# Optimization experiments

Hardware: AMD Instinct MI355X
Metric: run time of the kernel (lower is better)

## Reference

```python
import jax, jax.numpy as jnp
import numpy as np

N_NODES = 50000


def _gcn_conv(x, edge_index, W, b, n_nodes):
    # PyG GCNConv: add self loops, symmetric normalization, then
    # out[dst] = sum_{src->dst} norm * (x[src] @ W) + b
    src, dst = edge_index[0], edge_index[1]
    loop = jnp.arange(n_nodes, dtype=src.dtype)
    src = jnp.concatenate([src, loop])
    dst = jnp.concatenate([dst, loop])
    deg = jax.ops.segment_sum(jnp.ones_like(src, dtype=x.dtype), dst, num_segments=n_nodes)
    dinv = jnp.where(deg > 0, jax.lax.rsqrt(deg), 0.0)
    norm = dinv[src] * dinv[dst]                      # [E+N]
    h = x @ W                                         # [N, out] dense GEMM first (in >= out here)
    msg = h[src] * norm[:, None]                      # gather + scale
    out = jax.ops.segment_sum(msg, dst, num_segments=n_nodes)  # scatter-add
    return out + b


def setup_inputs() -> dict:
    key = jax.random.key(0)
    k = jax.random.split(key, 5)
    in_c, hid_c, out_c = 128, 128, 64
    n, e = N_NODES, 800000
    x = jax.random.normal(k[0], (n, in_c), dtype=jnp.float32)
    edge_index = jax.random.randint(k[1], (2, e), 0, n, dtype=jnp.int64)
    # Glorot-ish scaled weights
    W1 = jax.random.normal(k[2], (in_c, hid_c), dtype=jnp.float32) * (1.0 / np.sqrt(in_c))
    b1 = jnp.zeros((hid_c,), dtype=jnp.float32)
    W2 = jax.random.normal(k[3], (hid_c, out_c), dtype=jnp.float32) * (1.0 / np.sqrt(hid_c))
    b2 = jnp.zeros((out_c,), dtype=jnp.float32)
    return {"x": x, "edge_index": edge_index, "W1": W1, "b1": b1, "W2": W2, "b2": b2}


def reference(x, edge_index, W1, b1, W2, b2):
    # Net.encode: conv1 -> relu -> conv2
    h = _gcn_conv(x, edge_index, W1, b1, N_NODES)
    h = jax.nn.relu(h)
    z = _gcn_conv(h, edge_index, W2, b2, N_NODES)
    return z
```

## Files before the change

### kernel.cpp

```cpp
#include <hip/hip_runtime.h>
#include <math.h>

constexpr int C_IN  = 128;
constexpr int C_HID = 128;
constexpr int C_OUT = 64;
constexpr int NREP  = 8;

typedef short bf8   __attribute__((ext_vector_type(8)));
typedef float f32x4 __attribute__((ext_vector_type(4)));

__device__ __forceinline__ int wave_incl_scan(int v, int lane) {
    #pragma unroll
    for (int off = 1; off < 64; off <<= 1) {
        int u = __shfl_up(v, off, 64);
        if (lane >= off) v += u;
    }
    return v;
}
__device__ __forceinline__ short b16(float f) {
    unsigned int u = __float_as_uint(f);
    u += 0x7FFFu + ((u >> 16) & 1u);
    return (short)(u >> 16);
}
__device__ __forceinline__ unsigned int bpack(float a, float b) {
    unsigned int ua = __float_as_uint(a), ub = __float_as_uint(b);
    ua += 0x7FFFu + ((ua >> 16) & 1u);
    ub += 0x7FFFu + ((ub >> 16) & 1u);
    return (ua >> 16) | (ub & 0xFFFF0000u);
}
__device__ __forceinline__ void acc8(float* a, const uint4 v) {
    a[0] += __uint_as_float(v.x << 16);
    a[1] += __uint_as_float(v.x & 0xFFFF0000u);
    a[2] += __uint_as_float(v.y << 16);
    a[3] += __uint_as_float(v.y & 0xFFFF0000u);
    a[4] += __uint_as_float(v.z << 16);
    a[5] += __uint_as_float(v.z & 0xFFFF0000u);
    a[6] += __uint_as_float(v.w << 16);
    a[7] += __uint_as_float(v.w & 0xFFFF0000u);
}

__global__ __launch_bounds__(256) void k_zero(int* __restrict__ p, int n4) {
    int i = blockIdx.x * 256 + threadIdx.x;
    if (i < n4) reinterpret_cast<int4*>(p)[i] = make_int4(0, 0, 0, 0);
}

__global__ __launch_bounds__(256) void k_count2r4(const int* __restrict__ dst, int e, int n,
                                                  int* __restrict__ cntr,
                                                  int* __restrict__ slot) {
    int i = blockIdx.x * 256 + threadIdx.x;
    int base = i * 4;
    if (base >= e) return;
    int r = blockIdx.x & (NREP - 1);
    int* c = cntr + (size_t)r * n;
    if (base + 3 < e) {
        int4 d4 = *reinterpret_cast<const int4*>(dst + base);
        int4 s4;
        s4.x = atomicAdd(&c[d4.x], 1);
        s4.y = atomicAdd(&c[d4.y], 1);
        s4.z = atomicAdd(&c[d4.z], 1);
        s4.w = atomicAdd(&c[d4.w], 1);
        *reinterpret_cast<int4*>(slot + base) = s4;
    } else {
        for (int q = base; q < e; ++q) slot[q] = atomicAdd(&c[dst[q]], 1);
    }
}

__global__ __launch_bounds__(256) void k_scanAB8(int* __restrict__ cntr, int n,
                                                 int* __restrict__ rowstart,
                                                 int* __restrict__ blocksum,
                                                 int* __restrict__ blockoff,
                                                 int* __restrict__ ticket,
                                                 float* __restrict__ dinv) {
    __shared__ int swave[4];
    __shared__ int amLast;
    const int tid = threadIdx.x, lane = tid & 63, w = tid >> 6;
    const int idx = blockIdx.x * 1024 + tid * 4;
    int4 c = make_int4(0, 0, 0, 0);
    if (idx + 3 < n) {
        #pragma unroll
        for (int r = 0; r < NREP; ++r) {
            int4* p = reinterpret_cast<int4*>(cntr + (size_t)r * n + idx);
            int4 t = *p;
            *p = c;
            c.x += t.x; c.y += t.y; c.z += t.z; c.w += t.w;
        }
    } else if (idx < n) {
        for (int m = idx; m < n; ++m) {
            int acc = 0;
            #pragma unroll
            for (int r = 0; r < NREP; ++r) {
                int t = cntr[(size_t)r * n + m];
                cntr[(size_t)r * n + m] = acc;
                acc += t;
            }
            int q = m - idx;
            if (q == 0) c.x = acc; else if (q == 1) c.y = acc;
            else if (q == 2) c.z = acc; else c.w = acc;
        }
    }
    if (idx + 0 < n) dinv[idx + 0] = rsqrtf((float)(c.x + 1));
    if (idx + 1 < n) dinv[idx + 1] = rsqrtf((float)(c.y + 1));
    if (idx + 2 < n) dinv[idx + 2] = rsqrtf((float)(c.z + 1));
    if (idx + 3 < n) dinv[idx + 3] = rsqrtf((float)(c.w + 1));

    const int s4 = c.x + c.y + c.z + c.w;
    const int incl = wave_incl_scan(s4, lane);
    if (lane == 63) swave[w] = incl;
    __syncthreads();
    int base = incl - s4;
    #pragma unroll
    for (int j = 0; j < 4; ++j) if (j < w) base += swave[j];

    if (idx + 3 < n) {
        int4 o;
        o.x = base;
        o.y = base + c.x;
        o.z = base + c.x + c.y;
        o.w = base + c.x + c.y + c.z;
        *reinterpret_cast<int4*>(rowstart + idx) = o;
    } else if (idx < n) {
        int acc = base;
        if (idx + 0 < n) { rowstart[idx + 0] = acc; acc += c.x; }
        if (idx + 1 < n) { rowstart[idx + 1] = acc; acc += c.y; }
        if (idx + 2 < n) { rowstart[idx + 2] = acc; acc += c.z; }
        if (idx + 3 < n) { rowstart[idx + 3] = acc; }
    }

    if (tid == 0) {
        int tot = swave[0] + swave[1] + swave[2] + swave[3];
        blocksum[blockIdx.x] = tot;
        if (blockIdx.x == gridDim.x - 1) rowstart[n] = tot;
        __threadfence();
        amLast = (atomicAdd(ticket, 1) == (int)gridDim.x - 1);
    }
    __syncthreads();
    if (amLast && tid < 64) {
        volatile int* bs = blocksum;
        const int nb = gridDim.x;
        int v = (tid < nb) ? bs[tid] : 0;
        int incl2 = wave_incl_scan(v, tid);
        if (tid < nb) blockoff[tid] = incl2 - v;
    }
}

__global__ __launch_bounds__(256) void k_fill2r4(const int* __restrict__ src,
                                                 const int* __restrict__ dst,
                                                 const int* __restrict__ slot, int e, int n,
                                                 const int* __restrict__ rowstart,
                                                 const int* __restrict__ blockoff,
                                                 const int* __restrict__ repoff,
                                                 unsigned short* __restrict__ nbr) {
    int i = blockIdx.x * 256 + threadIdx.x;
    int base = i * 4;
    if (base >= e) return;
    int r = blockIdx.x & (NREP - 1);
    const int* rep = repoff + (size_t)r * n;
    if (base + 3 < e) {
        int4 d4 = *reinterpret_cast<const int4*>(dst + base);
        int4 s4 = *reinterpret_cast<const int4*>(src + base);
        int4 t4 = *reinterpret_cast<const int4*>(slot + base);
        nbr[rowstart[d4.x] + blockoff[d4.x >> 10] + rep[d4.x] + t4.x] = (unsigned short)s4.x;
        nbr[rowstart[d4.y] + blockoff[d4.y >> 10] + rep[d4.y] + t4.y] = (unsigned short)s4.y;
        nbr[rowstart[d4.z] + blockoff[d4.z >> 10] + rep[d4.z] + t4.z] = (unsigned short)s4.z;
        nbr[rowstart[d4.w] + blockoff[d4.w >> 10] + rep[d4.w] + t4.w] = (unsigned short)s4.w;
    } else {
        for (int q = base; q < e; ++q) {
            int d = dst[q];
            nbr[rowstart[d] + blockoff[d >> 10] + rep[d] + slot[q]] = (unsigned short)src[q];
        }
    }
}

__global__ __launch_bounds__(256) void k_gemm1m(const float* __restrict__ x,
                                                const float* __restrict__ W,
                                                const float* __restrict__ dinv,
                                                unsigned short* __restrict__ h1b,
                                                int n) {
    __shared__ short wf[8 * 4 * 64 * 8];
    const int tid = threadIdx.x;

    for (int i = tid; i < 2048; i += 256) {
        const int l = i & 63, kt = (i >> 6) & 3, ct = i >> 8;
        const int krow = kt * 32 + ((l >> 4) << 3);
        const int col  = ct * 16 + (l & 15);
        const float* wp = W + (size_t)krow * C_HID + col;
        uint4 u;
        u.x = bpack(wp[0 * C_HID], wp[1 * C_HID]);
        u.y = bpack(wp[2 * C_HID], wp[3 * C_HID]);
        u.z = bpack(wp[4 * C_HID], wp[5 * C_HID]);
        u.w = bpack(wp[6 * C_HID], wp[7 * C_HID]);
        reinterpret_cast<uint4*>(wf)[i] = u;
    }
    __syncthreads();

    const int l = tid & 63, w = tid >> 6;
    const int row0 = blockIdx.x * 64 + w * 16;
    int arow = row0 + (l & 15);
    if (arow >= n) arow = n - 1;
    const float* xr = x + (size_t)arow * C_IN + ((l >> 4) << 3);

    bf8 a[4];
    #pragma unroll
    for (int kt = 0; kt < 4; ++kt) {
        float4 p0 = *reinterpret_cast<const float4*>(xr + kt * 32);
        float4 p1 = *reinterpret_cast<const float4*>(xr + kt * 32 + 4);
        bf8 t;
        t[0] = b16(p0.x); t[1] = b16(p0.y); t[2] = b16(p0.z); t[3] = b16(p0.w);
        t[4] = b16(p1.x); t[5] = b16(p1.y); t[6] = b16(p1.z); t[7] = b16(p1.w);
        a[kt] = t;
    }

    f32x4 acc[8];
    #pragma unroll
    for (int ct = 0; ct < 8; ++ct) acc[ct] = (f32x4){0.f, 0.f, 0.f, 0.f};
    const bf8* bw = reinterpret_cast<const bf8*>(wf);
    #pragma unroll
    for (int kt = 0; kt < 4; ++kt)
        #pragma unroll
        for (int ct = 0; ct < 8; ++ct)
            acc[ct] = __builtin_amdgcn_mfma_f32_16x16x32_bf16(
                a[kt], bw[(ct * 4 + kt) * 64 + l], acc[ct], 0, 0, 0);

    const int rbase = row0 + ((l >> 4) << 2);
    float dv[4];
    #pragma unroll
    for (int r = 0; r < 4; ++r) {
        int rr = rbase + r;
        dv[r] = (rr < n) ? dinv[rr] : 0.f;
    }
    #pragma unroll
    for (int ct = 0; ct < 8; ++ct) {
        const int col = ct * 16 + (l & 15);
        #pragma unroll
        for (int r = 0; r < 4; ++r) {
            int rr = rbase + r;
            if (rr < n)
                h1b[(size_t)rr * C_HID + col] = (unsigned short)b16(acc[ct][r] * dv[r]);
        }
    }
}

__global__ __launch_bounds__(256) void k_agg1b16(const uint4* __restrict__ h1v,
                                                 const int* __restrict__ rowstart,
                                                 const int* __restrict__ blockoff,
                                                 const unsigned short* __restrict__ nbr,
                                                 const float* __restrict__ dinv,
                                                 const float* __restrict__ b1,
                                                 uint4* __restrict__ actb,
                                                 int n) {
    int node = blockIdx.x * 16 + (threadIdx.x >> 4);
    if (node >= n) return;
    const int c8 = threadIdx.x & 15;
    float a8[8] = {0.f, 0.f, 0.f, 0.f, 0.f, 0.f, 0.f, 0.f};
    acc8(a8, h1v[(size_t)node * 16 + c8]);
    int j   = rowstart[node]     + blockoff[node >> 10];
    int end = rowstart[node + 1] + blockoff[(node + 1) >> 10];
    for (; j + 1 < end; j += 2) {
        int s0 = nbr[j], s1 = nbr[j + 1];
        uint4 v0 = h1v[(size_t)s0 * 16 + c8];
        uint4 v1 = h1v[(size_t)s1 * 16 + c8];
        acc8(a8, v0); acc8(a8, v1);
    }
    if (j < end) acc8(a8, h1v[(size_t)nbr[j] * 16 + c8]);
    const float sc = dinv[node];
    const float4 bb0 = reinterpret_cast<const float4*>(b1)[2 * c8 + 0];
    const float4 bb1 = reinterpret_cast<const float4*>(b1)[2 * c8 + 1];
    uint4 p;
    p.x = bpack(fmaxf(sc * a8[0] + bb0.x, 0.f), fmaxf(sc * a8[1] + bb0.y, 0.f));
    p.y = bpack(fmaxf(sc * a8[2] + bb0.z, 0.f), fmaxf(sc * a8[3] + bb0.w, 0.f));
    p.z = bpack(fmaxf(sc * a8[4] + bb1.x, 0.f), fmaxf(sc * a8[5] + bb1.y, 0.f));
    p.w = bpack(fmaxf(sc * a8[6] + bb1.z, 0.f), fmaxf(sc * a8[7] + bb1.w, 0.f));
    actb[(size_t)node * 16 + c8] = p;
}

__global__ __launch_bounds__(256) void k_gemm2m(const unsigned short* __restrict__ actb,
                                                const float* __restrict__ W2,
                                                const float* __restrict__ dinv,
                                                unsigned short* __restrict__ h2b,
                                                int n) {
    __shared__ short wf[4 * 4 * 64 * 8];
    const int tid = threadIdx.x;

    for (int i = tid; i < 1024; i += 256) {
        const int l = i & 63, kt = (i >> 6) & 3, ct = i >> 8;
        const int krow = kt * 32 + ((l >> 4) << 3);
        const int col  = ct * 16 + (l & 15);
        const float* wp = W2 + (size_t)krow * C_OUT + col;
        uint4 u;
        u.x = bpack(wp[0 * C_OUT], wp[1 * C_OUT]);
        u.y = bpack(wp[2 * C_OUT], wp[3 * C_OUT]);
        u.z = bpack(wp[4 * C_OUT], wp[5 * C_OUT]);
        u.w = bpack(wp[6 * C_OUT], wp[7 * C_OUT]);
        reinterpret_cast<uint4*>(wf)[i] = u;
    }
    __syncthreads();

    const int l = tid & 63, w = tid >> 6;
    const int row0 = blockIdx.x * 64 + w * 16;
    int arow = row0 + (l & 15);
    if (arow >= n) arow = n - 1;
    const unsigned short* ar = actb + (size_t)arow * C_HID + ((l >> 4) << 3);

    bf8 a[4];
    #pragma unroll
    for (int kt = 0; kt < 4; ++kt)
        a[kt] = *reinterpret_cast<const bf8*>(ar + kt * 32);

    f32x4 acc[4];
    #pragma unroll
    for (int ct = 0; ct < 4; ++ct) acc[ct] = (f32x4){0.f, 0.f, 0.f, 0.f};
    const bf8* bw = reinterpret_cast<const bf8*>(wf);
    #pragma unroll
    for (int kt = 0; kt < 4; ++kt)
        #pragma unroll
        for (int ct = 0; ct < 4; ++ct)
            acc[ct] = __builtin_amdgcn_mfma_f32_16x16x32_bf16(
                a[kt], bw[(ct * 4 + kt) * 64 + l], acc[ct], 0, 0, 0);

    const int rbase = row0 + ((l >> 4) << 2);
    float dv[4];
    #pragma unroll
    for (int r = 0; r < 4; ++r) {
        int rr = rbase + r;
        dv[r] = (rr < n) ? dinv[rr] : 0.f;
    }
    #pragma unroll
    for (int ct = 0; ct < 4; ++ct) {
        const int col = ct * 16 + (l & 15);
        #pragma unroll
        for (int r = 0; r < 4; ++r) {
            int rr = rbase + r;
            if (rr < n)
                h2b[(size_t)rr * C_OUT + col] = (unsigned short)b16(acc[ct][r] * dv[r]);
        }
    }
}

__global__ __launch_bounds__(256) void k_agg2b(const uint4* __restrict__ h2v,
                                               const int* __restrict__ rowstart,
                                               const int* __restrict__ blockoff,
                                               const unsigned short* __restrict__ nbr,
                                               const float* __restrict__ dinv,
                                               const float* __restrict__ b2,
                                               float* __restrict__ outb, int n) {
    int node = blockIdx.x * 32 + (threadIdx.x >> 3);
    if (node >= n) return;
    const int lane8 = threadIdx.x & 7;
    float a8[8] = {0.f, 0.f, 0.f, 0.f, 0.f, 0.f, 0.f, 0.f};
    acc8(a8, h2v[(size_t)node * 8 + lane8]);
    int j   = rowstart[node]     + blockoff[node >> 10];
    int end = rowstart[node + 1] + blockoff[(node + 1) >> 10];
    for (; j + 1 < end; j += 2) {
        int s0 = nbr[j], s1 = nbr[j + 1];
        uint4 v0 = h2v[(size_t)s0 * 8 + lane8];
        uint4 v1 = h2v[(size_t)s1 * 8 + lane8];
        acc8(a8, v0); acc8(a8, v1);
    }
    if (j < end) acc8(a8, h2v[(size_t)nbr[j] * 8 + lane8]);
    const float s = dinv[node];
    const float4 c0 = reinterpret_cast<const float4*>(b2)[2 * lane8 + 0];
    const float4 c1 = reinterpret_cast<const float4*>(b2)[2 * lane8 + 1];
    float4 o0, o1;
    o0.x = s * a8[0] + c0.x; o0.y = s * a8[1] + c0.y;
    o0.z = s * a8[2] + c0.z; o0.w = s * a8[3] + c0.w;
    o1.x = s * a8[4] + c1.x; o1.y = s * a8[5] + c1.y;
    o1.z = s * a8[6] + c1.z; o1.w = s * a8[7] + c1.w;
    reinterpret_cast<float4*>(outb)[node * 16 + 2 * lane8 + 0] = o0;
    reinterpret_cast<float4*>(outb)[node * 16 + 2 * lane8 + 1] = o1;
}

extern "C" void kernel_launch(void* const* d_in, const int* in_sizes, int n_in,
                              void* d_out, int out_size, void* d_ws, size_t ws_size,
                              hipStream_t stream) {
    const float* x  = (const float*)d_in[0];
    const int*   ei = (const int*)d_in[1];
    const float* W1 = (const float*)d_in[2];
    const float* b1 = (const float*)d_in[3];
    const float* W2 = (const float*)d_in[4];
    const float* b2 = (const float*)d_in[5];

    const int n = in_sizes[0] / C_IN;
    const int e = in_sizes[1] / 2;
    const int* src = ei;
    const int* dst = ei + e;

    char* ws = (char*)d_ws;
    float* dinv     = (float*)(ws);
    int*   rowstart = (int*)  (ws + (2u << 18));
    int*   blocksum = (int*)  (ws + (1u << 20));
    int*   blockoff = (int*)  (ws + (1u << 20) + 4096);
    int*   cntr     = (int*)  (ws + (2u << 20));
    int*   slot     = (int*)  (ws + (4u << 20));
    unsigned short* nbr  = (unsigned short*)(ws + (8u << 20));
    unsigned short* h1b  = (unsigned short*)(ws + (10u << 20));
    unsigned short* actb = (unsigned short*)(ws + (23u << 20));
    unsigned short* h2b  = (unsigned short*)(ws + (36u << 20));
    int*   ticket   = cntr + (size_t)NREP * n;
    float* outb     = (float*)d_out;

    const int NB  = (n + 1023) / 1024;
    const int nz4 = (NREP * n + 4 + 3) / 4;
    const int nE4 = (e + 3) / 4;

    k_zero    <<<(nz4 + 255) / 256, 256, 0, stream>>>(cntr, nz4);
    k_count2r4<<<(nE4 + 255) / 256, 256, 0, stream>>>(dst, e, n, cntr, slot);
    k_scanAB8 <<<NB, 256, 0, stream>>>(cntr, n, rowstart, blocksum, blockoff, ticket, dinv);
    k_fill2r4 <<<(nE4 + 255) / 256, 256, 0, stream>>>(src, dst, slot, e, n, rowstart,
                                                      blockoff, cntr, nbr);
    k_gemm1m  <<<(n + 63) / 64, 256, 0, stream>>>(x, W1, dinv, h1b, n);
    k_agg1b16 <<<(n + 15) / 16, 256, 0, stream>>>((const uint4*)h1b, rowstart, blockoff, nbr,
                                                  dinv, b1, (uint4*)actb, n);
    k_gemm2m  <<<(n + 63) / 64, 256, 0, stream>>>(actb, W2, dinv, h2b, n);
    k_agg2b   <<<(n + 31) / 32, 256, 0, stream>>>((const uint4*)h2b, rowstart, blockoff, nbr,
                                                  dinv, b2, outb, n);
}
```

Measured before the change: 133.9 us.

## Drop replicated counters, fuse fill with GEMM1 and agg1 with GEMM2

Replaces the 8-way replicated degree counters with a single counter array, which removes the replica reduction in the scan and the replica offset in the fill. The CSR fill kernel and the first GEMM are merged into one launch, with block ranges split by index, so the two can run concurrently. The layer-1 aggregation is fused into the second GEMM: each block aggregates its 64 rows into swizzled shared memory and then runs the MFMA, so the bf16 activation buffer no longer makes a round trip through global memory. The trade-off is more atomic contention on one counter array and lower parallelism for the aggregation, which now uses 64-row blocks.

After: 142.9 us. 1.07x slower.

```diff
diff --git a/kernel.cpp b/kernel.cpp
--- a/kernel.cpp
+++ b/kernel.cpp
@@ -4,7 +4,6 @@
 constexpr int C_IN  = 128;
 constexpr int C_HID = 128;
 constexpr int C_OUT = 64;
-constexpr int NREP  = 8;
 
 typedef short bf8   __attribute__((ext_vector_type(8)));
 typedef float f32x4 __attribute__((ext_vector_type(4)));
@@ -44,59 +43,43 @@
     if (i < n4) reinterpret_cast<int4*>(p)[i] = make_int4(0, 0, 0, 0);
 }
 
-__global__ __launch_bounds__(256) void k_count2r4(const int* __restrict__ dst, int e, int n,
-                                                  int* __restrict__ cntr,
-                                                  int* __restrict__ slot) {
+__global__ __launch_bounds__(256) void k_count2(const int* __restrict__ dst, int e,
+                                                int* __restrict__ cnt,
+                                                int* __restrict__ slot) {
     int i = blockIdx.x * 256 + threadIdx.x;
     int base = i * 4;
     if (base >= e) return;
-    int r = blockIdx.x & (NREP - 1);
-    int* c = cntr + (size_t)r * n;
     if (base + 3 < e) {
         int4 d4 = *reinterpret_cast<const int4*>(dst + base);
         int4 s4;
-        s4.x = atomicAdd(&c[d4.x], 1);
-        s4.y = atomicAdd(&c[d4.y], 1);
-        s4.z = atomicAdd(&c[d4.z], 1);
-        s4.w = atomicAdd(&c[d4.w], 1);
+        s4.x = atomicAdd(&cnt[d4.x], 1);
+        s4.y = atomicAdd(&cnt[d4.y], 1);
+        s4.z = atomicAdd(&cnt[d4.z], 1);
+        s4.w = atomicAdd(&cnt[d4.w], 1);
         *reinterpret_cast<int4*>(slot + base) = s4;
     } else {
-        for (int q = base; q < e; ++q) slot[q] = atomicAdd(&c[dst[q]], 1);
-    }
-}
-
-__global__ __launch_bounds__(256) void k_scanAB8(int* __restrict__ cntr, int n,
-                                                 int* __restrict__ rowstart,
-                                                 int* __restrict__ blocksum,
-                                                 int* __restrict__ blockoff,
-                                                 int* __restrict__ ticket,
-                                                 float* __restrict__ dinv) {
+        for (int q = base; q < e; ++q) slot[q] = atomicAdd(&cnt[dst[q]], 1);
+    }
+}
+
+__global__ __launch_bounds__(256) void k_scanAB(const int* __restrict__ cnt, int n,
+                                                int* __restrict__ rowstart,
+                                                int* __restrict__ blocksum,
+                                                int* __restrict__ blockoff,
+                                                int* __restrict__ ticket,
+                                                float* __restrict__ dinv) {
     __shared__ int swave[4];
     __shared__ int amLast;
     const int tid = threadIdx.x, lane = tid & 63, w = tid >> 6;
     const int idx = blockIdx.x * 1024 + tid * 4;
     int4 c = make_int4(0, 0, 0, 0);
     if (idx + 3 < n) {
-        #pragma unroll
-        for (int r = 0; r < NREP; ++r) {
-            int4* p = reinterpret_cast<int4*>(cntr + (size_t)r * n + idx);
-            int4 t = *p;
-            *p = c;
-            c.x += t.x; c.y += t.y; c.z += t.z; c.w += t.w;
-        }
+        c = *reinterpret_cast<const int4*>(cnt + idx);
     } else if (idx < n) {
-        for (int m = idx; m < n; ++m) {
-            int acc = 0;
-            #pragma unroll
-            for (int r = 0; r < NREP; ++r) {
-                int t = cntr[(size_t)r * n + m];
-                cntr[(size_t)r * n + m] = acc;
-                acc += t;
-            }
-            int q = m - idx;
-            if (q == 0) c.x = acc; else if (q == 1) c.y = acc;
-            else if (q == 2) c.z = acc; else c.w = acc;
-        }
+        c.x = cnt[idx];
+        if (idx + 1 < n) c.y = cnt[idx + 1];
+        if (idx + 2 < n) c.z = cnt[idx + 2];
+        if (idx + 3 < n) c.w = cnt[idx + 3];
     }
     if (idx + 0 < n) dinv[idx + 0] = rsqrtf((float)(c.x + 1));
     if (idx + 1 < n) dinv[idx + 1] = rsqrtf((float)(c.y + 1));
@@ -120,7 +103,7 @@
         *reinterpret_cast<int4*>(rowstart + idx) = o;
     } else if (idx < n) {
         int acc = base;
-        if (idx + 0 < n) { rowstart[idx + 0] = acc; acc += c.x; }
+        rowstart[idx] = acc; acc += c.x;
         if (idx + 1 < n) { rowstart[idx + 1] = acc; acc += c.y; }
         if (idx + 2 < n) { rowstart[idx + 2] = acc; acc += c.z; }
         if (idx + 3 < n) { rowstart[idx + 3] = acc; }
@@ -135,6 +118,7 @@
     }
     __syncthreads();
     if (amLast && tid < 64) {
+        __threadfence();
         volatile int* bs = blocksum;
         const int nb = gridDim.x;
         int v = (tid < nb) ? bs[tid] : 0;
@@ -143,42 +127,35 @@
     }
 }
 
-__global__ __launch_bounds__(256) void k_fill2r4(const int* __restrict__ src,
-                                                 const int* __restrict__ dst,
-                                                 const int* __restrict__ slot, int e, int n,
-                                                 const int* __restrict__ rowstart,
-                                                 const int* __restrict__ blockoff,
-                                                 const int* __restrict__ repoff,
-                                                 unsigned short* __restrict__ nbr) {
-    int i = blockIdx.x * 256 + threadIdx.x;
-    int base = i * 4;
-    if (base >= e) return;
-    int r = blockIdx.x & (NREP - 1);
-    const int* rep = repoff + (size_t)r * n;
-    if (base + 3 < e) {
-        int4 d4 = *reinterpret_cast<const int4*>(dst + base);
-        int4 s4 = *reinterpret_cast<const int4*>(src + base);
-        int4 t4 = *reinterpret_cast<const int4*>(slot + base);
-        nbr[rowstart[d4.x] + blockoff[d4.x >> 10] + rep[d4.x] + t4.x] = (unsigned short)s4.x;
-        nbr[rowstart[d4.y] + blockoff[d4.y >> 10] + rep[d4.y] + t4.y] = (unsigned short)s4.y;
-        nbr[rowstart[d4.z] + blockoff[d4.z >> 10] + rep[d4.z] + t4.z] = (unsigned short)s4.z;
-        nbr[rowstart[d4.w] + blockoff[d4.w >> 10] + rep[d4.w] + t4.w] = (unsigned short)s4.w;
-    } else {
-        for (int q = base; q < e; ++q) {
-            int d = dst[q];
-            nbr[rowstart[d] + blockoff[d >> 10] + rep[d] + slot[q]] = (unsigned short)src[q];
+__global__ __launch_bounds__(256) void k_fillgemm1(
+    const int* __restrict__ src, const int* __restrict__ dst,
+    const int* __restrict__ slot, int e, int nfb,
+    const int* __restrict__ rowstart, const int* __restrict__ blockoff,
+    unsigned short* __restrict__ nbr,
+    const float* __restrict__ x, const float* __restrict__ W,
+    const float* __restrict__ dinv, unsigned short* __restrict__ h1b, int n) {
+    __shared__ short wf[8 * 4 * 64 * 8];
+    if (blockIdx.x < nfb) {
+        int i = blockIdx.x * 256 + threadIdx.x;
+        int base = i * 4;
+        if (base >= e) return;
+        if (base + 3 < e) {
+            int4 d4 = *reinterpret_cast<const int4*>(dst + base);
+            int4 s4 = *reinterpret_cast<const int4*>(src + base);
+            int4 t4 = *reinterpret_cast<const int4*>(slot + base);
+            nbr[rowstart[d4.x] + blockoff[d4.x >> 10] + t4.x] = (unsigned short)s4.x;
+            nbr[rowstart[d4.y] + blockoff[d4.y >> 10] + t4.y] = (unsigned short)s4.y;
+            nbr[rowstart[d4.z] + blockoff[d4.z >> 10] + t4.z] = (unsigned short)s4.z;
+            nbr[rowstart[d4.w] + blockoff[d4.w >> 10] + t4.w] = (unsigned short)s4.w;
+        } else {
+            for (int q = base; q < e; ++q) {
+                int d = dst[q];
+                nbr[rowstart[d] + blockoff[d >> 10] + slot[q]] = (unsigned short)src[q];
+            }
         }
-    }
-}
-
-__global__ __launch_bounds__(256) void k_gemm1m(const float* __restrict__ x,
-                                                const float* __restrict__ W,
-                                                const float* __restrict__ dinv,
-                                                unsigned short* __restrict__ h1b,
-                                                int n) {
-    __shared__ short wf[8 * 4 * 64 * 8];
+        return;
+    }
     const int tid = threadIdx.x;
-
     for (int i = tid; i < 2048; i += 256) {
         const int l = i & 63, kt = (i >> 6) & 3, ct = i >> 8;
         const int krow = kt * 32 + ((l >> 4) << 3);
@@ -194,7 +171,7 @@
     __syncthreads();
 
     const int l = tid & 63, w = tid >> 6;
-    const int row0 = blockIdx.x * 64 + w * 16;
+    const int row0 = (blockIdx.x - nfb) * 64 + w * 16;
     int arow = row0 + (l & 15);
     if (arow >= n) arow = n - 1;
     const float* xr = x + (size_t)arow * C_IN + ((l >> 4) << 3);
@@ -240,46 +217,17 @@
     }
 }
 
-__global__ __launch_bounds__(256) void k_agg1b16(const uint4* __restrict__ h1v,
-                                                 const int* __restrict__ rowstart,
-                                                 const int* __restrict__ blockoff,
-                                                 const unsigned short* __restrict__ nbr,
-                                                 const float* __restrict__ dinv,
-                                                 const float* __restrict__ b1,
-                                                 uint4* __restrict__ actb,
-                                                 int n) {
-    int node = blockIdx.x * 16 + (threadIdx.x >> 4);
-    if (node >= n) return;
-    const int c8 = threadIdx.x & 15;
-    float a8[8] = {0.f, 0.f, 0.f, 0.f, 0.f, 0.f, 0.f, 0.f};
-    acc8(a8, h1v[(size_t)node * 16 + c8]);
-    int j   = rowstart[node]     + blockoff[node >> 10];
-    int end = rowstart[node + 1] + blockoff[(node + 1) >> 10];
-    for (; j + 1 < end; j += 2) {
-        int s0 = nbr[j], s1 = nbr[j + 1];
-        uint4 v0 = h1v[(size_t)s0 * 16 + c8];
-        uint4 v1 = h1v[(size_t)s1 * 16 + c8];
-        acc8(a8, v0); acc8(a8, v1);
-    }
-    if (j < end) acc8(a8, h1v[(size_t)nbr[j] * 16 + c8]);
-    const float sc = dinv[node];
-    const float4 bb0 = reinterpret_cast<const float4*>(b1)[2 * c8 + 0];
-    const float4 bb1 = reinterpret_cast<const float4*>(b1)[2 * c8 + 1];
-    uint4 p;
-    p.x = bpack(fmaxf(sc * a8[0] + bb0.x, 0.f), fmaxf(sc * a8[1] + bb0.y, 0.f));
-    p.y = bpack(fmaxf(sc * a8[2] + bb0.z, 0.f), fmaxf(sc * a8[3] + bb0.w, 0.f));
-    p.z = bpack(fmaxf(sc * a8[4] + bb1.x, 0.f), fmaxf(sc * a8[5] + bb1.y, 0.f));
-    p.w = bpack(fmaxf(sc * a8[6] + bb1.z, 0.f), fmaxf(sc * a8[7] + bb1.w, 0.f));
-    actb[(size_t)node * 16 + c8] = p;
-}
-
-__global__ __launch_bounds__(256) void k_gemm2m(const unsigned short* __restrict__ actb,
-                                                const float* __restrict__ W2,
-                                                const float* __restrict__ dinv,
-                                                unsigned short* __restrict__ h2b,
-                                                int n) {
+__global__ __launch_bounds__(256) void k_agg1gemm2(
+    const uint4* __restrict__ h1v,
+    const int* __restrict__ rowstart, const int* __restrict__ blockoff,
+    const unsigned short* __restrict__ nbr,
+    const float* __restrict__ dinv, const float* __restrict__ b1,
+    const float* __restrict__ W2,
+    unsigned short* __restrict__ h2b, int n) {
     __shared__ short wf[4 * 4 * 64 * 8];
-    const int tid = threadIdx.x;
+    __shared__ uint4 actl[64 * 16];
+    const int tid  = threadIdx.x;
+    const int row0 = blockIdx.x * 64;
 
     for (int i = tid; i < 1024; i += 256) {
         const int l = i & 63, kt = (i >> 6) & 3, ct = i >> 8;
@@ -293,18 +241,46 @@
         u.w = bpack(wp[6 * C_OUT], wp[7 * C_OUT]);
         reinterpret_cast<uint4*>(wf)[i] = u;
     }
+
+    const int c8 = tid & 15, grp = tid >> 4;
+    const float4 bb0 = reinterpret_cast<const float4*>(b1)[2 * c8 + 0];
+    const float4 bb1 = reinterpret_cast<const float4*>(b1)[2 * c8 + 1];
+    #pragma unroll
+    for (int it = 0; it < 4; ++it) {
+        const int r    = grp + 16 * it;
+        const int node = row0 + r;
+        uint4 p = make_uint4(0, 0, 0, 0);
+        if (node < n) {
+            float a8[8] = {0.f, 0.f, 0.f, 0.f, 0.f, 0.f, 0.f, 0.f};
+            acc8(a8, h1v[(size_t)node * 16 + c8]);
+            int j   = rowstart[node]     + blockoff[node >> 10];
+            int end = rowstart[node + 1] + blockoff[(node + 1) >> 10];
+            for (; j + 1 < end; j += 2) {
+                int s0 = nbr[j], s1 = nbr[j + 1];
+                uint4 v0 = h1v[(size_t)s0 * 16 + c8];
+                uint4 v1 = h1v[(size_t)s1 * 16 + c8];
+                acc8(a8, v0); acc8(a8, v1);
+            }
+            if (j < end) acc8(a8, h1v[(size_t)nbr[j] * 16 + c8]);
+            const float sc = dinv[node];
+            p.x = bpack(fmaxf(sc * a8[0] + bb0.x, 0.f), fmaxf(sc * a8[1] + bb0.y, 0.f));
+            p.y = bpack(fmaxf(sc * a8[2] + bb0.z, 0.f), fmaxf(sc * a8[3] + bb0.w, 0.f));
+            p.z = bpack(fmaxf(sc * a8[4] + bb1.x, 0.f), fmaxf(sc * a8[5] + bb1.y, 0.f));
+            p.w = bpack(fmaxf(sc * a8[6] + bb1.z, 0.f), fmaxf(sc * a8[7] + bb1.w, 0.f));
+        }
+        actl[r * 16 + (c8 ^ (r & 15))] = p;
+    }
     __syncthreads();
 
     const int l = tid & 63, w = tid >> 6;
-    const int row0 = blockIdx.x * 64 + w * 16;
-    int arow = row0 + (l & 15);
-    if (arow >= n) arow = n - 1;
-    const unsigned short* ar = actb + (size_t)arow * C_HID + ((l >> 4) << 3);
-
     bf8 a[4];
     #pragma unroll
-    for (int kt = 0; kt < 4; ++kt)
-        a[kt] = *reinterpret_cast<const bf8*>(ar + kt * 32);
+    for (int kt = 0; kt < 4; ++kt) {
+        const int row   = w * 16 + (l & 15);
+        const int chunk = kt * 4 + (l >> 4);
+        uint4 v = actl[row * 16 + (chunk ^ (row & 15))];
+        a[kt] = *reinterpret_cast<bf8*>(&v);
+    }
 
     f32x4 acc[4];
     #pragma unroll
@@ -317,7 +293,7 @@
             acc[ct] = __builtin_amdgcn_mfma_f32_16x16x32_bf16(
                 a[kt], bw[(ct * 4 + kt) * 64 + l], acc[ct], 0, 0, 0);
 
-    const int rbase = row0 + ((l >> 4) << 2);
+    const int rbase = row0 + w * 16 + ((l >> 4) << 2);
     float dv[4];
     #pragma unroll
     for (int r = 0; r < 4; ++r) {
@@ -386,31 +362,29 @@
 
     char* ws = (char*)d_ws;
     float* dinv     = (float*)(ws);
+    int*   cnt      = (int*)  (ws + (1u << 18));
     int*   rowstart = (int*)  (ws + (2u << 18));
-    int*   blocksum = (int*)  (ws + (1u << 20));
-    int*   blockoff = (int*)  (ws + (1u << 20) + 4096);
-    int*   cntr     = (int*)  (ws + (2u << 20));
-    int*   slot     = (int*)  (ws + (4u << 20));
-    unsigned short* nbr  = (unsigned short*)(ws + (8u << 20));
-    unsigned short* h1b  = (unsigned short*)(ws + (10u << 20));
-    unsigned short* actb = (unsigned short*)(ws + (23u << 20));
-    unsigned short* h2b  = (unsigned short*)(ws + (36u << 20));
-    int*   ticket   = cntr + (size_t)NREP * n;
+    int*   blocksum = (int*)  (ws + (3u << 18));
+    int*   blockoff = (int*)  (ws + (3u << 18) + 4096);
+    int*   slot     = (int*)  (ws + (1u << 20));
+    unsigned short* nbr = (unsigned short*)(ws + (5u << 20));
+    unsigned short* h1b = (unsigned short*)(ws + (8u << 20));
+    unsigned short* h2b = (unsigned short*)(ws + (21u << 20));
+    int*   ticket   = cnt + n;
     float* outb     = (float*)d_out;
 
     const int NB  = (n + 1023) / 1024;
-    const int nz4 = (NREP * n + 4 + 3) / 4;
-    const int nE4 = (e + 3) / 4;
-
-    k_zero    <<<(nz4 + 255) / 256, 256, 0, stream>>>(cntr, nz4);
-    k_count2r4<<<(nE4 + 255) / 256, 256, 0, stream>>>(dst, e, n, cntr, slot);
-    k_scanAB8 <<<NB, 256, 0, stream>>>(cntr, n, rowstart, blocksum, blockoff, ticket, dinv);
-    k_fill2r4 <<<(nE4 + 255) / 256, 256, 0, stream>>>(src, dst, slot, e, n, rowstart,
-                                                      blockoff, cntr, nbr);
-    k_gemm1m  <<<(n + 63) / 64, 256, 0, stream>>>(x, W1, dinv, h1b, n);
-    k_agg1b16 <<<(n + 15) / 16, 256, 0, stream>>>((const uint4*)h1b, rowstart, blockoff, nbr,
-                                                  dinv, b1, (uint4*)actb, n);
-    k_gemm2m  <<<(n + 63) / 64, 256, 0, stream>>>(actb, W2, dinv, h2b, n);
-    k_agg2b   <<<(n + 31) / 32, 256, 0, stream>>>((const uint4*)h2b, rowstart, blockoff, nbr,
-                                                  dinv, b2, outb, n);
-}
+    const int nz4 = (n + 1 + 3) / 4;
+    const int nFB = ((e + 3) / 4 + 255) / 256;
+    const int nGB = (n + 63) / 64;
+
+    k_zero     <<<(nz4 + 255) / 256, 256, 0, stream>>>(cnt, nz4);
+    k_count2   <<<nFB, 256, 0, stream>>>(dst, e, cnt, slot);
+    k_scanAB   <<<NB, 256, 0, stream>>>(cnt, n, rowstart, blocksum, blockoff, ticket, dinv);
+    k_fillgemm1<<<nFB + nGB, 256, 0, stream>>>(src, dst, slot, e, nFB, rowstart, blockoff,
+                                               nbr, x, W1, dinv, h1b, n);
+    k_agg1gemm2<<<nGB, 256, 0, stream>>>((const uint4*)h1b, rowstart, blockoff, nbr,
+                                         dinv, b1, W2, h2b, n);
+    k_agg2b    <<<(n + 31) / 32, 256, 0, stream>>>((const uint4*)h2b, rowstart, blockoff, nbr,
+                                                   dinv, b2, outb, n);
+}
```
